# Kernel tuning notes

Measured on AMD Instinct MI355X. Metric: run time of the kernel, lower is better.

## Reference

```python
import jax, jax.numpy as jnp
import numpy as np

B, S, D, H = 4, 1024, 1024, 16
DK = D // H  # d_k = 64

def setup_inputs() -> dict:
    key = jax.random.key(0)
    ks = jax.random.split(key, 6)
    sc = 0.02
    return {
        "x": jax.random.normal(ks[0], (B, S, D), jnp.float32),
        "bias": jax.random.normal(ks[1], (H, S, S), jnp.float32),
        "Wq": jax.random.normal(ks[2], (D, D), jnp.float32) * sc,
        "Wk": jax.random.normal(ks[3], (D, D), jnp.float32) * sc,
        "Wv": jax.random.normal(ks[4], (D, D), jnp.float32) * sc,
        "Wo": jax.random.normal(ks[5], (D, D), jnp.float32) * sc,
    }

def _split_heads(t):
    # [B,S,D] -> [B,H,S,DK]
    b, s, _ = t.shape
    return t.reshape(b, s, H, DK).transpose(0, 2, 1, 3)

def reference(x, bias, Wq, Wk, Wv, Wo):
    q = _split_heads(x @ Wq)
    k = _split_heads(x @ Wk)
    v = _split_heads(x @ Wv)
    scale = jnp.asarray(DK, x.dtype) ** 0.5
    # [B,H,S,S] scores with additive per-head bias (broadcast over batch)
    attn = jnp.einsum('bhqd,bhkd->bhqk', q / scale, k) + bias[None]
    attn = jax.nn.softmax(attn, axis=-1)
    ctx = jnp.einsum('bhqk,bhkd->bhqd', attn, v)
    ctx = ctx.transpose(0, 2, 1, 3).reshape(x.shape[0], x.shape[1], -1)
    out = ctx @ Wo
    return (out, attn)
```

## Files before the change

kernel.cpp:

```cpp
#include <hip/hip_runtime.h>
#include <hip/hip_bf16.h>


typedef __bf16 bf16_t;
typedef __bf16 bf16x4 __attribute__((ext_vector_type(4)));
typedef __bf16 bf16x8 __attribute__((ext_vector_type(8)));
typedef float f32x4 __attribute__((ext_vector_type(4)));

#define MFMA16(a, b, c) __builtin_amdgcn_mfma_f32_16x16x32_bf16(a, b, c, 0, 0, 0)

__global__ __launch_bounds__(256) void cast_f32_bf16(const float* __restrict__ in,
                                                     bf16_t* __restrict__ out, int n4) {
    int i = blockIdx.x * blockDim.x + threadIdx.x;
    if (i >= n4) return;
    float4 v = reinterpret_cast<const float4*>(in)[i];
    bf16x4 o = { (bf16_t)v.x, (bf16_t)v.y, (bf16_t)v.z, (bf16_t)v.w };
    reinterpret_cast<bf16x4*>(out)[i] = o;
}

__global__ __launch_bounds__(1024) void transpose_cast_w(const float* __restrict__ w0,
                                                         const float* __restrict__ w1,
                                                         const float* __restrict__ w2,
                                                         const float* __restrict__ w3,
                                                         bf16_t* __restrict__ wt) {
    __shared__ float tile[32][33];
    const float* src = (blockIdx.z == 0) ? w0 : (blockIdx.z == 1) ? w1
                     : (blockIdx.z == 2) ? w2 : w3;
    bf16_t* dst = wt + (size_t)blockIdx.z * 1024 * 1024;
    int r0 = blockIdx.y * 32, c0 = blockIdx.x * 32;
    tile[threadIdx.y][threadIdx.x] = src[(size_t)(r0 + threadIdx.y) * 1024 + c0 + threadIdx.x];
    __syncthreads();
    dst[(size_t)(c0 + threadIdx.y) * 1024 + r0 + threadIdx.x] = (bf16_t)tile[threadIdx.x][threadIdx.y];
}

#define GEMM_BODY(A, BT)                                                                 \
    __shared__ bf16_t As[128 * 32];                                                      \
    __shared__ bf16_t Bs[128 * 32];                                                      \
    const int tid = threadIdx.x;                                                         \
    const int lane = tid & 63, wave = tid >> 6;                                          \
    const int lr = lane & 15, lg = lane >> 4;                                            \
    const int m_base = blockIdx.x * 128, n_base = blockIdx.y * 128;                      \
    const int wm = (wave >> 1) * 64, wn = (wave & 1) * 64;                               \
    const int srow = tid >> 1;                                                           \
    const int sl0 = (tid & 1) * 2;                                                       \
    const int sl1 = sl0 + 1;                                                             \
    const int off0 = srow * 32 + ((sl0 ^ ((srow >> 1) & 3)) * 8);                        \
    const int off1 = srow * 32 + ((sl1 ^ ((srow >> 1) & 3)) * 8);                        \
    const bf16_t* aptr = (A) + (size_t)(m_base + srow) * 1024 + sl0 * 8;                 \
    const bf16_t* bptr = (BT) + (size_t)(n_base + srow) * 1024 + sl0 * 8;                \
    bf16x8 ra0 = *reinterpret_cast<const bf16x8*>(aptr);                                 \
    bf16x8 ra1 = *reinterpret_cast<const bf16x8*>(aptr + 8);                             \
    bf16x8 rb0 = *reinterpret_cast<const bf16x8*>(bptr);                                 \
    bf16x8 rb1 = *reinterpret_cast<const bf16x8*>(bptr + 8);                             \
    f32x4 acc[4][4] = {};                                                                \
    for (int kb = 32; kb <= 1024; kb += 32) {                                            \
        __syncthreads();                                                                 \
        *reinterpret_cast<bf16x8*>(&As[off0]) = ra0;                                     \
        *reinterpret_cast<bf16x8*>(&As[off1]) = ra1;                                     \
        *reinterpret_cast<bf16x8*>(&Bs[off0]) = rb0;                                     \
        *reinterpret_cast<bf16x8*>(&Bs[off1]) = rb1;                                     \
        if (kb < 1024) {                                                                 \
            ra0 = *reinterpret_cast<const bf16x8*>(aptr + kb);                           \
            ra1 = *reinterpret_cast<const bf16x8*>(aptr + kb + 8);                       \
            rb0 = *reinterpret_cast<const bf16x8*>(bptr + kb);                           \
            rb1 = *reinterpret_cast<const bf16x8*>(bptr + kb + 8);                       \
        }                                                                                \
        __syncthreads();                                                                 \
        bf16x8 af[4], bfr[4];                                                            \
        _Pragma("unroll") for (int i = 0; i < 4; ++i) {                                  \
            const int row = wm + i * 16 + lr;                                            \
            af[i] = *reinterpret_cast<const bf16x8*>(                                    \
                &As[row * 32 + ((lg ^ ((row >> 1) & 3)) * 8)]);                          \
        }                                                                                \
        _Pragma("unroll") for (int j = 0; j < 4; ++j) {                                  \
            const int row = wn + j * 16 + lr;                                            \
            bfr[j] = *reinterpret_cast<const bf16x8*>(                                   \
                &Bs[row * 32 + ((lg ^ ((row >> 1) & 3)) * 8)]);                          \
        }                                                                                \
        _Pragma("unroll") for (int i = 0; i < 4; ++i)                                    \
            _Pragma("unroll") for (int j = 0; j < 4; ++j)                                \
                acc[i][j] = MFMA16(af[i], bfr[j], acc[i][j]);                            \
    }

__global__ __launch_bounds__(256, 3) void gemm_qkv(const bf16_t* __restrict__ A,
                                                   const bf16_t* __restrict__ wT,
                                                   bf16_t* __restrict__ qhp,
                                                   bf16_t* __restrict__ khp,
                                                   bf16_t* __restrict__ vp) {
    const int z = blockIdx.z;
    const bf16_t* BT = wT + ((size_t)z << 20);
    GEMM_BODY(A, BT)
    bf16_t* dst = (z == 0) ? qhp : (z == 1) ? khp : vp;
    const float scale = (z == 0) ? 0.125f : 1.0f;
#pragma unroll
    for (int i = 0; i < 4; ++i)
#pragma unroll
        for (int j = 0; j < 4; ++j)
#pragma unroll
            for (int r = 0; r < 4; ++r) {
                const int row = m_base + wm + i * 16 + lg * 4 + r;
                const int col = n_base + wn + j * 16 + lr;
                const float v = acc[i][j][r] * scale;
                const int b = row >> 10, s = row & 1023;
                const int h = col >> 6, d = col & 63;
                const size_t bh16 = (size_t)(b * 16 + h) << 16;
                if (z == 2)
                    dst[bh16 + ((s >> 5) << 11) + d * 32 + (s & 31)] = (bf16_t)v;
                else
                    dst[bh16 + ((d >> 5) << 15) + s * 32 + (d & 31)] = (bf16_t)v;
            }
}

__global__ __launch_bounds__(256, 3) void gemm_out(const bf16_t* __restrict__ A,
                                                   const bf16_t* __restrict__ BT,
                                                   float* __restrict__ out) {
    GEMM_BODY(A, BT)
#pragma unroll
    for (int i = 0; i < 4; ++i)
#pragma unroll
        for (int j = 0; j < 4; ++j)
#pragma unroll
            for (int r = 0; r < 4; ++r) {
                const int row = m_base + wm + i * 16 + lg * 4 + r;
                const int col = n_base + wn + j * 16 + lr;
                out[(size_t)row * 1024 + col] = acc[i][j][r];
            }
}

__global__ __launch_bounds__(256, 2) void fused_attn(const bf16_t* __restrict__ qhp,
                                                     const bf16_t* __restrict__ khp,
                                                     const bf16_t* __restrict__ vp,
                                                     const float* __restrict__ bias,
                                                     float* __restrict__ attn,
                                                     bf16_t* __restrict__ ctxb) {
    __shared__ float ftile[4][16][256];
    __shared__ float smaxp[64];
    __shared__ float ssump[64];
    const int lane = threadIdx.x & 63;
    const int wave = threadIdx.x >> 6;
    const int lr = lane & 15, lg = lane >> 4;

    const int g = blockIdx.x;
    const int j = g >> 3;
    const int h = (g & 7) + 8 * (j >> 8);
    const int qt = (j & 255) >> 2;
    const int b = j & 3;
    const int bh = b * 16 + h;
    const int m0 = qt * 16;

    const bf16_t* qbase = qhp + ((size_t)bh << 16);
    const bf16x8 aq0 = *reinterpret_cast<const bf16x8*>(qbase + (m0 + lr) * 32 + lg * 8);
    const bf16x8 aq1 = *reinterpret_cast<const bf16x8*>(qbase + 32768 + (m0 + lr) * 32 + lg * 8);

    const int c0 = wave * 256;
    const bf16_t* kp0 = khp + ((size_t)bh << 16) + (size_t)(c0 + lr) * 32 + lg * 8;

    char* tw = reinterpret_cast<char*>(&ftile[wave][0][0]);
    const int myswz = (lr & 7) << 4;

    bf16x8 kfA[16];
#pragma unroll
    for (int f = 0; f < 16; ++f)
        kfA[f] = *reinterpret_cast<const bf16x8*>(kp0 + f * 512);

    {
        const float* bbase = bias + ((size_t)h << 20) + (size_t)m0 * 1024 + c0;
#pragma unroll
        for (int i = 0; i < 16; ++i) {
            const int co = (lane * 4) ^ ((i & 7) * 4);
            f32x4 bv = *reinterpret_cast<const f32x4*>(bbase + (size_t)i * 1024 + co);
            *reinterpret_cast<f32x4*>(tw + i * 1024 + lane * 16) = bv;
        }
    }

    f32x4 acc[16];
#pragma unroll
    for (int f = 0; f < 16; ++f)
        acc[f] = *reinterpret_cast<const f32x4*>(tw + lr * 1024 + ((f * 64 + lg * 16) ^ myswz));

#pragma unroll
    for (int f = 0; f < 16; ++f)
        acc[f] = MFMA16(kfA[f], aq0, acc[f]);
    {
        bf16x8 kfB[16];
#pragma unroll
        for (int f = 0; f < 16; ++f)
            kfB[f] = *reinterpret_cast<const bf16x8*>(kp0 + 32768 + f * 512);
#pragma unroll
        for (int f = 0; f < 16; ++f)
            acc[f] = MFMA16(kfB[f], aq1, acc[f]);
    }

    f32x4 m4 = acc[0];
#pragma unroll
    for (int f = 1; f < 16; ++f) {
#pragma unroll
        for (int r = 0; r < 4; ++r) m4[r] = fmaxf(m4[r], acc[f][r]);
    }
    float mx = fmaxf(fmaxf(m4[0], m4[1]), fmaxf(m4[2], m4[3]));
    mx = fmaxf(mx, __shfl_xor(mx, 16));
    mx = fmaxf(mx, __shfl_xor(mx, 32));
    if (lane < 16) smaxp[wave * 16 + lr] = mx;
    __syncthreads();
    const float gm = fmaxf(fmaxf(smaxp[lr], smaxp[16 + lr]),
                           fmaxf(smaxp[32 + lr], smaxp[48 + lr]));

    f32x4 s4 = {0.f, 0.f, 0.f, 0.f};
#pragma unroll
    for (int f = 0; f < 16; ++f) {
#pragma unroll
        for (int r = 0; r < 4; ++r) {
            const float e = __expf(acc[f][r] - gm);
            acc[f][r] = e;
            s4[r] += e;
        }
    }
    float sm = (s4[0] + s4[1]) + (s4[2] + s4[3]);
    sm += __shfl_xor(sm, 16);
    sm += __shfl_xor(sm, 32);
    if (lane < 16) ssump[wave * 16 + lr] = sm;
    __syncthreads();
    const float invl = 1.0f / (ssump[lr] + ssump[16 + lr] + ssump[32 + lr] + ssump[48 + lr]);

    const bf16_t* vpb = vp + ((size_t)bh << 16) + (size_t)(wave * 8) * 2048 + lr * 32 + lg * 8;
    bf16x8 vf0[4][4];
#pragma unroll
    for (int ks = 0; ks < 4; ++ks)
#pragma unroll
        for (int f2 = 0; f2 < 4; ++f2)
            vf0[ks][f2] = *reinterpret_cast<const bf16x8*>(vpb + ks * 2048 + f2 * 512);

#pragma unroll
    for (int f = 0; f < 16; ++f) {
        f32x4 v = acc[f];
#pragma unroll
        for (int r = 0; r < 4; ++r) v[r] *= invl;
        *reinterpret_cast<f32x4*>(tw + lr * 1024 + ((f * 64 + lg * 16) ^ myswz)) = v;
    }

    {
        float* obase = attn + ((size_t)bh << 20) + (size_t)m0 * 1024 + c0;
#pragma unroll
        for (int i = 0; i < 16; ++i) {
            const int co = (lane * 4) ^ ((i & 7) * 4);
            f32x4 v = *reinterpret_cast<const f32x4*>(tw + i * 1024 + lane * 16);
            *reinterpret_cast<f32x4*>(obase + (size_t)i * 1024 + co) = v;
        }
    }

    f32x4 cacc[4];
#pragma unroll
    for (int f2 = 0; f2 < 4; ++f2) cacc[f2] = (f32x4){0.f, 0.f, 0.f, 0.f};

    bf16x8 vf1[4][4];
#pragma unroll
    for (int ks = 0; ks < 4; ++ks)
#pragma unroll
        for (int f2 = 0; f2 < 4; ++f2)
            vf1[ks][f2] = *reinterpret_cast<const bf16x8*>(vpb + (4 + ks) * 2048 + f2 * 512);

#pragma unroll
    for (int ks = 0; ks < 8; ++ks) {
        f32x4 p0 = *reinterpret_cast<const f32x4*>(
            tw + lr * 1024 + ((ks * 128 + lg * 32) ^ myswz));
        f32x4 p1 = *reinterpret_cast<const f32x4*>(
            tw + lr * 1024 + ((ks * 128 + lg * 32 + 16) ^ myswz));
        bf16x8 pa = { (bf16_t)p0[0], (bf16_t)p0[1], (bf16_t)p0[2], (bf16_t)p0[3],
                      (bf16_t)p1[0], (bf16_t)p1[1], (bf16_t)p1[2], (bf16_t)p1[3] };
#pragma unroll
        for (int f2 = 0; f2 < 4; ++f2)
            cacc[f2] = MFMA16(pa, (ks < 4) ? vf0[ks & 3][f2] : vf1[ks & 3][f2], cacc[f2]);
    }

    float* credw = &ftile[wave][0][0];
#pragma unroll
    for (int f2 = 0; f2 < 4; ++f2)
#pragma unroll
        for (int r = 0; r < 4; ++r)
            credw[(lg * 4 + r) * 64 + f2 * 16 + lr] = cacc[f2][r];
    __syncthreads();
    const int row_l = wave * 4 + lg;
    const int dk0 = lr * 4;
    f32x4 s0 = *reinterpret_cast<const f32x4*>(&ftile[0][0][0] + row_l * 64 + dk0);
    f32x4 s1 = *reinterpret_cast<const f32x4*>(&ftile[1][0][0] + row_l * 64 + dk0);
    f32x4 s2 = *reinterpret_cast<const f32x4*>(&ftile[2][0][0] + row_l * 64 + dk0);
    f32x4 s3 = *reinterpret_cast<const f32x4*>(&ftile[3][0][0] + row_l * 64 + dk0);
    f32x4 st = (s0 + s1) + (s2 + s3);
    bf16x4 o4 = { (bf16_t)st[0], (bf16_t)st[1], (bf16_t)st[2], (bf16_t)st[3] };
    *reinterpret_cast<bf16x4*>(
        &ctxb[(size_t)(b * 1024 + m0 + row_l) * 1024 + h * 64 + dk0]) = o4;
}

extern "C" void kernel_launch(void* const* d_in, const int* in_sizes, int n_in,
                              void* d_out, int out_size, void* d_ws, size_t ws_size,
                              hipStream_t stream) {
    const float* x    = (const float*)d_in[0];
    const float* bias = (const float*)d_in[1];
    const float* Wq   = (const float*)d_in[2];
    const float* Wk   = (const float*)d_in[3];
    const float* Wv   = (const float*)d_in[4];
    const float* Wo   = (const float*)d_in[5];
    float* out  = (float*)d_out;
    float* attn = out + (size_t)4 * 1024 * 1024;

    char* ws = (char*)d_ws;
    bf16_t* xb   = (bf16_t*)(ws);
    bf16_t* wT   = (bf16_t*)(ws + ((size_t)8 << 20));
    bf16_t* qhp  = (bf16_t*)(ws + ((size_t)16 << 20));
    bf16_t* khp  = (bf16_t*)(ws + ((size_t)24 << 20));
    bf16_t* vp   = (bf16_t*)(ws + ((size_t)32 << 20));
    bf16_t* ctxb = (bf16_t*)(ws + ((size_t)40 << 20));
    bf16_t* woT = wT + ((size_t)3 << 20);

    cast_f32_bf16<<<dim3(4096), dim3(256), 0, stream>>>(x, xb, 1024 * 1024);
    transpose_cast_w<<<dim3(32, 32, 4), dim3(32, 32), 0, stream>>>(Wq, Wk, Wv, Wo, wT);

    gemm_qkv<<<dim3(32, 8, 3), dim3(256), 0, stream>>>(xb, wT, qhp, khp, vp);

    fused_attn<<<dim3(4096), dim3(256), 0, stream>>>(qhp, khp, vp, bias, attn, ctxb);

    gemm_out<<<dim3(32, 8), dim3(256), 0, stream>>>(ctxb, woT, out);
}
```

Baseline: 202.8 us.

## Process 32 query rows per attention block to reuse K/V fragments

Each fused attention block now handles two 16-row query tiles instead of one, halving the grid. Every loaded K and V fragment feeds MFMAs for both tiles, which cuts K/V reload traffic per block. Probabilities are now staged in LDS as bf16 rather than fp32, and the attention output is written from those bf16-rounded values, which shrinks LDS use but lowers the precision of the returned attention matrix. The two accumulator sets double register pressure and can reduce occupancy.

```diff
diff --git a/kernel.cpp b/kernel.cpp
--- a/kernel.cpp
+++ b/kernel.cpp
@@ -133,94 +133,127 @@
                                                      const float* __restrict__ bias,
                                                      float* __restrict__ attn,
                                                      bf16_t* __restrict__ ctxb) {
-    __shared__ float ftile[4][16][256];
-    __shared__ float smaxp[64];
-    __shared__ float ssump[64];
+    __shared__ f32x4 wlds4[4][1024];
+    __shared__ float smaxp[128];
+    __shared__ float ssump[128];
     const int lane = threadIdx.x & 63;
     const int wave = threadIdx.x >> 6;
     const int lr = lane & 15, lg = lane >> 4;
 
     const int g = blockIdx.x;
     const int j = g >> 3;
-    const int h = (g & 7) + 8 * (j >> 8);
-    const int qt = (j & 255) >> 2;
+    const int h = (g & 7) + 8 * (j >> 7);
+    const int qt = (j >> 2) & 31;
     const int b = j & 3;
     const int bh = b * 16 + h;
-    const int m0 = qt * 16;
+    const int m0 = qt * 32;
 
     const bf16_t* qbase = qhp + ((size_t)bh << 16);
-    const bf16x8 aq0 = *reinterpret_cast<const bf16x8*>(qbase + (m0 + lr) * 32 + lg * 8);
-    const bf16x8 aq1 = *reinterpret_cast<const bf16x8*>(qbase + 32768 + (m0 + lr) * 32 + lg * 8);
+    const bf16x8 aqA0 = *reinterpret_cast<const bf16x8*>(qbase + (m0 + lr) * 32 + lg * 8);
+    const bf16x8 aqA1 = *reinterpret_cast<const bf16x8*>(qbase + 32768 + (m0 + lr) * 32 + lg * 8);
+    const bf16x8 aqB0 = *reinterpret_cast<const bf16x8*>(qbase + (m0 + 16 + lr) * 32 + lg * 8);
+    const bf16x8 aqB1 = *reinterpret_cast<const bf16x8*>(qbase + 32768 + (m0 + 16 + lr) * 32 + lg * 8);
 
     const int c0 = wave * 256;
     const bf16_t* kp0 = khp + ((size_t)bh << 16) + (size_t)(c0 + lr) * 32 + lg * 8;
 
-    char* tw = reinterpret_cast<char*>(&ftile[wave][0][0]);
+    char* tw = reinterpret_cast<char*>(&wlds4[wave][0]);
     const int myswz = (lr & 7) << 4;
 
-    bf16x8 kfA[16];
+    const float* bb0 = bias + ((size_t)h << 20) + (size_t)m0 * 1024 + c0;
+#pragma unroll
+    for (int i = 0; i < 16; ++i) {
+        const int co = (lane * 4) ^ ((i & 7) * 4);
+        f32x4 bv = *reinterpret_cast<const f32x4*>(bb0 + (size_t)i * 1024 + co);
+        *reinterpret_cast<f32x4*>(tw + i * 1024 + lane * 16) = bv;
+    }
+    f32x4 acc0[16];
 #pragma unroll
     for (int f = 0; f < 16; ++f)
-        kfA[f] = *reinterpret_cast<const bf16x8*>(kp0 + f * 512);
-
-    {
-        const float* bbase = bias + ((size_t)h << 20) + (size_t)m0 * 1024 + c0;
-#pragma unroll
-        for (int i = 0; i < 16; ++i) {
-            const int co = (lane * 4) ^ ((i & 7) * 4);
-            f32x4 bv = *reinterpret_cast<const f32x4*>(bbase + (size_t)i * 1024 + co);
-            *reinterpret_cast<f32x4*>(tw + i * 1024 + lane * 16) = bv;
-        }
-    }
-
-    f32x4 acc[16];
+        acc0[f] = *reinterpret_cast<const f32x4*>(tw + lr * 1024 + ((f * 64 + lg * 16) ^ myswz));
+
+    const float* bb1 = bb0 + 16 * 1024;
+#pragma unroll
+    for (int i = 0; i < 16; ++i) {
+        const int co = (lane * 4) ^ ((i & 7) * 4);
+        f32x4 bv = *reinterpret_cast<const f32x4*>(bb1 + (size_t)i * 1024 + co);
+        *reinterpret_cast<f32x4*>(tw + i * 1024 + lane * 16) = bv;
+    }
+    f32x4 acc1[16];
 #pragma unroll
     for (int f = 0; f < 16; ++f)
-        acc[f] = *reinterpret_cast<const f32x4*>(tw + lr * 1024 + ((f * 64 + lg * 16) ^ myswz));
-
-#pragma unroll
-    for (int f = 0; f < 16; ++f)
-        acc[f] = MFMA16(kfA[f], aq0, acc[f]);
-    {
-        bf16x8 kfB[16];
-#pragma unroll
-        for (int f = 0; f < 16; ++f)
-            kfB[f] = *reinterpret_cast<const bf16x8*>(kp0 + 32768 + f * 512);
-#pragma unroll
-        for (int f = 0; f < 16; ++f)
-            acc[f] = MFMA16(kfB[f], aq1, acc[f]);
-    }
-
-    f32x4 m4 = acc[0];
+        acc1[f] = *reinterpret_cast<const f32x4*>(tw + lr * 1024 + ((f * 64 + lg * 16) ^ myswz));
+
+#pragma unroll
+    for (int half = 0; half < 2; ++half) {
+        const bf16x8 aqA = half ? aqA1 : aqA0;
+        const bf16x8 aqB = half ? aqB1 : aqB0;
+#pragma unroll
+        for (int bt = 0; bt < 2; ++bt) {
+            bf16x8 kf[8];
+#pragma unroll
+            for (int u = 0; u < 8; ++u)
+                kf[u] = *reinterpret_cast<const bf16x8*>(
+                    kp0 + half * 32768 + (bt * 8 + u) * 512);
+#pragma unroll
+            for (int u = 0; u < 8; ++u) {
+                acc0[bt * 8 + u] = MFMA16(kf[u], aqA, acc0[bt * 8 + u]);
+                acc1[bt * 8 + u] = MFMA16(kf[u], aqB, acc1[bt * 8 + u]);
+            }
+        }
+    }
+
+    f32x4 m40 = acc0[0], m41 = acc1[0];
 #pragma unroll
     for (int f = 1; f < 16; ++f) {
 #pragma unroll
-        for (int r = 0; r < 4; ++r) m4[r] = fmaxf(m4[r], acc[f][r]);
-    }
-    float mx = fmaxf(fmaxf(m4[0], m4[1]), fmaxf(m4[2], m4[3]));
-    mx = fmaxf(mx, __shfl_xor(mx, 16));
-    mx = fmaxf(mx, __shfl_xor(mx, 32));
-    if (lane < 16) smaxp[wave * 16 + lr] = mx;
+        for (int r = 0; r < 4; ++r) {
+            m40[r] = fmaxf(m40[r], acc0[f][r]);
+            m41[r] = fmaxf(m41[r], acc1[f][r]);
+        }
+    }
+    float mx0 = fmaxf(fmaxf(m40[0], m40[1]), fmaxf(m40[2], m40[3]));
+    float mx1 = fmaxf(fmaxf(m41[0], m41[1]), fmaxf(m41[2], m41[3]));
+    mx0 = fmaxf(mx0, __shfl_xor(mx0, 16));
+    mx0 = fmaxf(mx0, __shfl_xor(mx0, 32));
+    mx1 = fmaxf(mx1, __shfl_xor(mx1, 16));
+    mx1 = fmaxf(mx1, __shfl_xor(mx1, 32));
+    if (lane < 16) {
+        smaxp[wave * 16 + lr] = mx0;
+        smaxp[64 + wave * 16 + lr] = mx1;
+    }
     __syncthreads();
-    const float gm = fmaxf(fmaxf(smaxp[lr], smaxp[16 + lr]),
-                           fmaxf(smaxp[32 + lr], smaxp[48 + lr]));
-
-    f32x4 s4 = {0.f, 0.f, 0.f, 0.f};
+    const float gm0 = fmaxf(fmaxf(smaxp[lr], smaxp[16 + lr]),
+                            fmaxf(smaxp[32 + lr], smaxp[48 + lr]));
+    const float gm1 = fmaxf(fmaxf(smaxp[64 + lr], smaxp[80 + lr]),
+                            fmaxf(smaxp[96 + lr], smaxp[112 + lr]));
+
+    f32x4 s40 = {0.f, 0.f, 0.f, 0.f}, s41 = {0.f, 0.f, 0.f, 0.f};
 #pragma unroll
     for (int f = 0; f < 16; ++f) {
 #pragma unroll
         for (int r = 0; r < 4; ++r) {
-            const float e = __expf(acc[f][r] - gm);
-            acc[f][r] = e;
-            s4[r] += e;
-        }
-    }
-    float sm = (s4[0] + s4[1]) + (s4[2] + s4[3]);
-    sm += __shfl_xor(sm, 16);
-    sm += __shfl_xor(sm, 32);
-    if (lane < 16) ssump[wave * 16 + lr] = sm;
+            const float e0 = __expf(acc0[f][r] - gm0);
+            const float e1 = __expf(acc1[f][r] - gm1);
+            acc0[f][r] = e0;
+            acc1[f][r] = e1;
+            s40[r] += e0;
+            s41[r] += e1;
+        }
+    }
+    float sm0 = (s40[0] + s40[1]) + (s40[2] + s40[3]);
+    float sm1 = (s41[0] + s41[1]) + (s41[2] + s41[3]);
+    sm0 += __shfl_xor(sm0, 16);
+    sm0 += __shfl_xor(sm0, 32);
+    sm1 += __shfl_xor(sm1, 16);
+    sm1 += __shfl_xor(sm1, 32);
+    if (lane < 16) {
+        ssump[wave * 16 + lr] = sm0;
+        ssump[64 + wave * 16 + lr] = sm1;
+    }
     __syncthreads();
-    const float invl = 1.0f / (ssump[lr] + ssump[16 + lr] + ssump[32 + lr] + ssump[48 + lr]);
+    const float invl0 = 1.0f / (ssump[lr] + ssump[16 + lr] + ssump[32 + lr] + ssump[48 + lr]);
+    const float invl1 = 1.0f / (ssump[64 + lr] + ssump[80 + lr] + ssump[96 + lr] + ssump[112 + lr]);
 
     const bf16_t* vpb = vp + ((size_t)bh << 16) + (size_t)(wave * 8) * 2048 + lr * 32 + lg * 8;
     bf16x8 vf0[4][4];
@@ -232,26 +265,36 @@
 
 #pragma unroll
     for (int f = 0; f < 16; ++f) {
-        f32x4 v = acc[f];
-#pragma unroll
-        for (int r = 0; r < 4; ++r) v[r] *= invl;
-        *reinterpret_cast<f32x4*>(tw + lr * 1024 + ((f * 64 + lg * 16) ^ myswz)) = v;
+        f32x4 v0 = acc0[f], v1 = acc1[f];
+#pragma unroll
+        for (int r = 0; r < 4; ++r) { v0[r] *= invl0; v1[r] *= invl1; }
+        bf16x4 p0 = { (bf16_t)v0[0], (bf16_t)v0[1], (bf16_t)v0[2], (bf16_t)v0[3] };
+        bf16x4 p1 = { (bf16_t)v1[0], (bf16_t)v1[1], (bf16_t)v1[2], (bf16_t)v1[3] };
+        const int ro = lr * 512 + ((f * 32 + lg * 8) ^ myswz);
+        *reinterpret_cast<bf16x4*>(tw + ro) = p0;
+        *reinterpret_cast<bf16x4*>(tw + 8192 + ro) = p1;
     }
 
     {
         float* obase = attn + ((size_t)bh << 20) + (size_t)m0 * 1024 + c0;
 #pragma unroll
         for (int i = 0; i < 16; ++i) {
-            const int co = (lane * 4) ^ ((i & 7) * 4);
-            f32x4 v = *reinterpret_cast<const f32x4*>(tw + i * 1024 + lane * 16);
-            *reinterpret_cast<f32x4*>(obase + (size_t)i * 1024 + co) = v;
-        }
-    }
-
-    f32x4 cacc[4];
-#pragma unroll
-    for (int f2 = 0; f2 < 4; ++f2) cacc[f2] = (f32x4){0.f, 0.f, 0.f, 0.f};
-
+            const int cc = (lane * 4) ^ ((i & 7) * 8);
+            bf16x4 q0 = *reinterpret_cast<const bf16x4*>(tw + i * 512 + lane * 8);
+            bf16x4 q1 = *reinterpret_cast<const bf16x4*>(tw + 8192 + i * 512 + lane * 8);
+            f32x4 w0 = { (float)q0[0], (float)q0[1], (float)q0[2], (float)q0[3] };
+            f32x4 w1 = { (float)q1[0], (float)q1[1], (float)q1[2], (float)q1[3] };
+            *reinterpret_cast<f32x4*>(obase + (size_t)i * 1024 + cc) = w0;
+            *reinterpret_cast<f32x4*>(obase + (size_t)(16 + i) * 1024 + cc) = w1;
+        }
+    }
+
+    f32x4 cacc0[4], cacc1[4];
+#pragma unroll
+    for (int f2 = 0; f2 < 4; ++f2) {
+        cacc0[f2] = (f32x4){0.f, 0.f, 0.f, 0.f};
+        cacc1[f2] = (f32x4){0.f, 0.f, 0.f, 0.f};
+    }
     bf16x8 vf1[4][4];
 #pragma unroll
     for (int ks = 0; ks < 4; ++ks)
@@ -260,35 +303,56 @@
             vf1[ks][f2] = *reinterpret_cast<const bf16x8*>(vpb + (4 + ks) * 2048 + f2 * 512);
 
 #pragma unroll
-    for (int ks = 0; ks < 8; ++ks) {
-        f32x4 p0 = *reinterpret_cast<const f32x4*>(
-            tw + lr * 1024 + ((ks * 128 + lg * 32) ^ myswz));
-        f32x4 p1 = *reinterpret_cast<const f32x4*>(
-            tw + lr * 1024 + ((ks * 128 + lg * 32 + 16) ^ myswz));
-        bf16x8 pa = { (bf16_t)p0[0], (bf16_t)p0[1], (bf16_t)p0[2], (bf16_t)p0[3],
-                      (bf16_t)p1[0], (bf16_t)p1[1], (bf16_t)p1[2], (bf16_t)p1[3] };
+    for (int ks = 0; ks < 4; ++ks) {
+        const int po = lr * 512 + ((ks * 64 + lg * 16) ^ myswz);
+        bf16x8 pa0 = *reinterpret_cast<const bf16x8*>(tw + po);
+        bf16x8 pa1 = *reinterpret_cast<const bf16x8*>(tw + 8192 + po);
+#pragma unroll
+        for (int f2 = 0; f2 < 4; ++f2) {
+            cacc0[f2] = MFMA16(pa0, vf0[ks][f2], cacc0[f2]);
+            cacc1[f2] = MFMA16(pa1, vf0[ks][f2], cacc1[f2]);
+        }
+    }
+#pragma unroll
+    for (int ks = 4; ks < 8; ++ks) {
+        const int po = lr * 512 + ((ks * 64 + lg * 16) ^ myswz);
+        bf16x8 pa0 = *reinterpret_cast<const bf16x8*>(tw + po);
+        bf16x8 pa1 = *reinterpret_cast<const bf16x8*>(tw + 8192 + po);
+#pragma unroll
+        for (int f2 = 0; f2 < 4; ++f2) {
+            cacc0[f2] = MFMA16(pa0, vf1[ks - 4][f2], cacc0[f2]);
+            cacc1[f2] = MFMA16(pa1, vf1[ks - 4][f2], cacc1[f2]);
+        }
+    }
+
+    {
+        float* credw = reinterpret_cast<float*>(tw);
 #pragma unroll
         for (int f2 = 0; f2 < 4; ++f2)
-            cacc[f2] = MFMA16(pa, (ks < 4) ? vf0[ks & 3][f2] : vf1[ks & 3][f2], cacc[f2]);
-    }
-
-    float* credw = &ftile[wave][0][0];
-#pragma unroll
-    for (int f2 = 0; f2 < 4; ++f2)
-#pragma unroll
-        for (int r = 0; r < 4; ++r)
-            credw[(lg * 4 + r) * 64 + f2 * 16 + lr] = cacc[f2][r];
+#pragma unroll
+            for (int r = 0; r < 4; ++r) {
+                credw[(lg * 4 + r) * 64 + f2 * 16 + lr] = cacc0[f2][r];
+                credw[1024 + (lg * 4 + r) * 64 + f2 * 16 + lr] = cacc1[f2][r];
+            }
+    }
     __syncthreads();
     const int row_l = wave * 4 + lg;
     const int dk0 = lr * 4;
-    f32x4 s0 = *reinterpret_cast<const f32x4*>(&ftile[0][0][0] + row_l * 64 + dk0);
-    f32x4 s1 = *reinterpret_cast<const f32x4*>(&ftile[1][0][0] + row_l * 64 + dk0);
-    f32x4 s2 = *reinterpret_cast<const f32x4*>(&ftile[2][0][0] + row_l * 64 + dk0);
-    f32x4 s3 = *reinterpret_cast<const f32x4*>(&ftile[3][0][0] + row_l * 64 + dk0);
-    f32x4 st = (s0 + s1) + (s2 + s3);
-    bf16x4 o4 = { (bf16_t)st[0], (bf16_t)st[1], (bf16_t)st[2], (bf16_t)st[3] };
-    *reinterpret_cast<bf16x4*>(
-        &ctxb[(size_t)(b * 1024 + m0 + row_l) * 1024 + h * 64 + dk0]) = o4;
+#pragma unroll
+    for (int t = 0; t < 2; ++t) {
+        f32x4 s0 = *reinterpret_cast<const f32x4*>(
+            reinterpret_cast<const float*>(&wlds4[0][0]) + t * 1024 + row_l * 64 + dk0);
+        f32x4 s1 = *reinterpret_cast<const f32x4*>(
+            reinterpret_cast<const float*>(&wlds4[1][0]) + t * 1024 + row_l * 64 + dk0);
+        f32x4 s2 = *reinterpret_cast<const f32x4*>(
+            reinterpret_cast<const float*>(&wlds4[2][0]) + t * 1024 + row_l * 64 + dk0);
+        f32x4 s3 = *reinterpret_cast<const f32x4*>(
+            reinterpret_cast<const float*>(&wlds4[3][0]) + t * 1024 + row_l * 64 + dk0);
+        f32x4 st = (s0 + s1) + (s2 + s3);
+        bf16x4 o4 = { (bf16_t)st[0], (bf16_t)st[1], (bf16_t)st[2], (bf16_t)st[3] };
+        *reinterpret_cast<bf16x4*>(
+            &ctxb[(size_t)(b * 1024 + m0 + t * 16 + row_l) * 1024 + h * 64 + dk0]) = o4;
+    }
 }
 
 extern "C" void kernel_launch(void* const* d_in, const int* in_sizes, int n_in,
@@ -317,7 +381,7 @@
 
     gemm_qkv<<<dim3(32, 8, 3), dim3(256), 0, stream>>>(xb, wT, qhp, khp, vp);
 
-    fused_attn<<<dim3(4096), dim3(256), 0, stream>>>(qhp, khp, vp, bias, attn, ctxb);
+    fused_attn<<<dim3(2048), dim3(256), 0, stream>>>(qhp, khp, vp, bias, attn, ctxb);
 
     gemm_out<<<dim3(32, 8), dim3(256), 0, stream>>>(ctxb, woT, out);
 }
```

After: 180.8 us. 1.12x faster.
